# Performance work log

Measured on AMD Instinct MI355X. Metric: run time of the kernel, lower is better.

Reference implementation:

```python
import jax, jax.numpy as jnp
import numpy as np

N = 50000
P = 200000
L = 6
IN_DIM = 128
OUT_DIM = 128
HEADS = 4


def setup_inputs() -> dict:
    key = jax.random.key(0)
    ks = jax.random.split(key, 7)
    x = jax.random.normal(ks[0], (N, IN_DIM), dtype=jnp.float32)
    path_list = jax.random.randint(ks[1], (P, L), 0, N, dtype=jnp.int64)
    s = 0.1
    w_ih = jax.random.normal(ks[2], (3 * OUT_DIM, IN_DIM), dtype=jnp.float32) * s
    w_hh = jax.random.normal(ks[3], (3 * OUT_DIM, OUT_DIM), dtype=jnp.float32) * s
    b_ih = jax.random.normal(ks[4], (3 * OUT_DIM,), dtype=jnp.float32) * s
    b_hh = jax.random.normal(ks[5], (3 * OUT_DIM,), dtype=jnp.float32) * s
    a = jax.random.uniform(ks[6], (OUT_DIM, HEADS), dtype=jnp.float32) * 2.0 - 1.0
    return {"x": x, "path_list": path_list, "w_ih": w_ih, "w_hh": w_hh,
            "b_ih": b_ih, "b_hh": b_hh, "a": a}


def _gru_final_hidden(feats, w_ih, w_hh, b_ih, b_hh):
    # feats: [P, L, in_dim]; PyTorch GRU cell semantics, h0 = 0.
    out_dim = w_hh.shape[1]
    p = feats.shape[0]

    def step(h, xt):
        gi = xt @ w_ih.T + b_ih          # [P, 3*out]
        gh = h @ w_hh.T + b_hh           # [P, 3*out]
        ir, iz, i_n = jnp.split(gi, 3, axis=-1)
        hr, hz, h_n = jnp.split(gh, 3, axis=-1)
        r = jax.nn.sigmoid(ir + hr)
        z = jax.nn.sigmoid(iz + hz)
        n_cand = jnp.tanh(i_n + r * h_n)
        h_new = (1.0 - z) * n_cand + z * h
        return h_new, None

    h0 = jnp.zeros((p, out_dim), feats.dtype)
    xs = jnp.swapaxes(feats, 0, 1)       # [L, P, in_dim]
    h, _ = jax.lax.scan(step, h0, xs)
    return h                              # [P, out_dim]


def reference(x, path_list, w_ih, w_hh, b_ih, b_hh, a):
    n, out_dim = x.shape[0], w_hh.shape[1]
    heads = a.shape[1]
    # F.embedding(path_list, x): gather path features [P, L, in_dim]
    feats = x[path_list]
    path_emb = _gru_final_hidden(feats, w_ih, w_hh, b_ih, b_hh)       # [P, out]
    # unnormalized attention per head
    att_un = jnp.exp(jax.nn.leaky_relu(path_emb @ a, negative_slope=0.2))  # [P, H]
    row = path_list[:, -1]                                             # owner node of each path
    # M @ att_un : segment-sum over owner nodes
    att_sum = jax.ops.segment_sum(att_un, row, num_segments=n)         # [N, H]
    # M.t() @ (1/att_sum) : gather back to paths
    att_low = (1.0 / att_sum)[row]                                     # [P, H]
    att_n = att_un * att_low                                           # [P, H]
    # reshape(-1,1).repeat(1,out).reshape(P,-1): each head's scalar repeated out_dim times
    att_rep = jnp.repeat(att_n, out_dim, axis=1)                       # [P, H*out]
    emb_rep = jnp.tile(path_emb, (1, heads))                           # [P, H*out]
    path_att_emb = att_rep * emb_rep
    node_att_emb = jax.ops.segment_sum(path_att_emb, row, num_segments=n)  # [N, H*out]
    return node_att_emb
```

## Files before the change

### kernel.cpp

```cpp
#include <hip/hip_runtime.h>
#include <hip/hip_bf16.h>
#include <math.h>

#define NN 50000
#define PP 200000
#define LL 6
#define DD 128
#define HH 4

#define TM 64
#define NT 512
#define HPAD 132

typedef __attribute__((ext_vector_type(8))) short short8;
typedef __attribute__((ext_vector_type(4))) float f32x4;

__device__ __forceinline__ unsigned short f2bf(float v) {
    __hip_bfloat16 h = __float2bfloat16(v);
    return *(unsigned short*)&h;
}
__device__ __forceinline__ float bf2f(unsigned short u) {
    union { unsigned int i; float f; } c; c.i = ((unsigned int)u) << 16; return c.f;
}
__device__ __forceinline__ float fast_rcp(float x) { return __builtin_amdgcn_rcpf(x); }
__device__ __forceinline__ float fast_sigmoid(float x) {
    return fast_rcp(1.f + __expf(-x));
}
__device__ __forceinline__ float fast_tanh(float x) {
    float e = __expf(-2.f * fabsf(x));
    float t = (1.f - e) * fast_rcp(1.f + e);
    return copysignf(t, x);
}

__global__ void prep_x_kernel(const float* __restrict__ x,
                              unsigned short* __restrict__ xb) {
    int i = blockIdx.x * 256 + threadIdx.x;
    if (i < NN * DD) xb[i] = f2bf(x[i]);
}
__global__ void prep_w_kernel(const float* __restrict__ w_ih,
                              const float* __restrict__ w_hh,
                              unsigned short* __restrict__ wib,
                              unsigned short* __restrict__ whb) {
    int i = blockIdx.x * 256 + threadIdx.x;
    if (i < 3 * DD * DD) { wib[i] = f2bf(w_ih[i]); whb[i] = f2bf(w_hh[i]); }
}

__global__ void histo_kernel(const int* __restrict__ path_list,
                             int* __restrict__ cnt) {
    int p = blockIdx.x * 256 + threadIdx.x;
    if (p < PP) atomicAdd(&cnt[path_list[p * LL + (LL - 1)]], 1);
}

__global__ void scan_kernel(const int* __restrict__ cnt,
                            int* __restrict__ offs,
                            int* __restrict__ cursor) {
    __shared__ int ls[256];
    const int t = threadIdx.x;
    const int chunk = (NN + 255) / 256;
    int s = 0;
    for (int j = 0; j < chunk; ++j) {
        int i = t + j * 256;
        if (i < NN) s += cnt[i];
    }
    ls[t] = s; __syncthreads();
    for (int off = 1; off < 256; off <<= 1) {
        int v = (t >= off) ? ls[t - off] : 0;
        __syncthreads();
        ls[t] += v;
        __syncthreads();
    }
    int run = (t == 0) ? 0 : ls[t - 1];
    for (int j = 0; j < chunk; ++j) {
        int i = t + j * 256;
        if (i < NN) { offs[i] = run; cursor[i] = run; run += cnt[i]; }
    }
}

__global__ void scatter_kernel(const int* __restrict__ path_list,
                               int* __restrict__ cursor,
                               int* __restrict__ sorted) {
    int p = blockIdx.x * 256 + threadIdx.x;
    if (p < PP) {
        int row = path_list[p * LL + (LL - 1)];
        int k = atomicAdd(&cursor[row], 1);
        sorted[k] = p;
    }
}

__global__ __launch_bounds__(NT, 2)
void gru_att_kernel(const unsigned short* __restrict__ xb,
                    const int*   __restrict__ path_list,
                    const unsigned short* __restrict__ wib,
                    const unsigned short* __restrict__ whb,
                    const float* __restrict__ b_ih,
                    const float* __restrict__ b_hh,
                    const float* __restrict__ a,
                    float* __restrict__ att_sum,
                    unsigned short* __restrict__ emb,
                    float* __restrict__ att_un_g)
{
    __shared__ __align__(16) unsigned char smem[43520];
    unsigned short* hsb    = (unsigned short*)smem;
    unsigned short* xs     = (unsigned short*)(smem + 16384);
    float*          hs_f   = (float*)smem;
    float*          red_s  = (float*)(smem + 33792);
    int*            nodes_s= (int*)(smem + 41984);

    const int tid  = threadIdx.x;
    const int lane = tid & 63;
    const int wave = tid >> 6;
    const int lcol = lane & 15;
    const int quad = lane >> 4;
    const int d    = wave * 16 + lcol;
    const int p0   = blockIdx.x * TM;
    const int ko   = quad * 8;

    short8 Bx[3][4], Bh[3][4];
    #pragma unroll
    for (int c = 0; c < 3; ++c)
        #pragma unroll
        for (int ks = 0; ks < 4; ++ks) {
            Bx[c][ks] = *(const short8*)(wib + (size_t)(c * DD + d) * DD + ks * 32 + ko);
            Bh[c][ks] = *(const short8*)(whb + (size_t)(c * DD + d) * DD + ks * 32 + ko);
        }
    const float brz = b_ih[d]       + b_hh[d];
    const float bzz = b_ih[d + 128] + b_hh[d + 128];
    const float bin = b_ih[d + 256];
    const float bhn = b_hh[d + 256];

    for (int i = tid; i < TM * LL; i += NT) nodes_s[i] = path_list[(size_t)p0 * LL + i];
    for (int i = tid; i < TM * DD / 8; i += NT)
        ((uint4*)hsb)[i] = make_uint4(0u, 0u, 0u, 0u);

    float hreg[16];
    #pragma unroll
    for (int i = 0; i < 16; ++i) hreg[i] = 0.f;

    __syncthreads();

    const int gpi = tid >> 3;
    const int gtt = tid & 7;
    const int gpm = gpi & 15;

    uint4 xg0, xg1;
    {
        int node = nodes_s[gpi * LL + 0];
        const uint4* src = (const uint4*)(xb + (size_t)node * DD + gtt * 16);
        xg0 = src[0]; xg1 = src[1];
    }

    f32x4 accR[4], accZ[4], accN[4], accH[4];

    #pragma unroll
    for (int t = 0; t < LL; ++t) {
        {
            int kb0 = 2 * gtt, kb1 = 2 * gtt + 1;
            *(uint4*)(xs + gpi * DD + ((kb0 ^ gpm) * 8)) = xg0;
            *(uint4*)(xs + gpi * DD + ((kb1 ^ gpm) * 8)) = xg1;
        }
        __syncthreads();

        if (t < LL - 1) {
            int node = nodes_s[gpi * LL + t + 1];
            const uint4* src = (const uint4*)(xb + (size_t)node * DD + gtt * 16);
            xg0 = src[0]; xg1 = src[1];
        }

        #pragma unroll
        for (int rt = 0; rt < 4; ++rt) {
            accR[rt] = (f32x4){brz, brz, brz, brz};
            accZ[rt] = (f32x4){bzz, bzz, bzz, bzz};
            accN[rt] = (f32x4){bin, bin, bin, bin};
            accH[rt] = (f32x4){bhn, bhn, bhn, bhn};
        }

        #pragma unroll
        for (int ks = 0; ks < 4; ++ks) {
            const int kb = ks * 4 + quad;
            #pragma unroll
            for (int rt = 0; rt < 4; ++rt) {
                const int p = rt * 16 + lcol;
                short8 ax = *(const short8*)(xs  + p * DD + ((kb ^ lcol) * 8));
                short8 ah = *(const short8*)(hsb + p * DD + ((kb ^ lcol) * 8));
                accR[rt] = __builtin_amdgcn_mfma_f32_16x16x32_bf16(ax, Bx[0][ks], accR[rt], 0, 0, 0);
                accZ[rt] = __builtin_amdgcn_mfma_f32_16x16x32_bf16(ax, Bx[1][ks], accZ[rt], 0, 0, 0);
                accN[rt] = __builtin_amdgcn_mfma_f32_16x16x32_bf16(ax, Bx[2][ks], accN[rt], 0, 0, 0);
                accR[rt] = __builtin_amdgcn_mfma_f32_16x16x32_bf16(ah, Bh[0][ks], accR[rt], 0, 0, 0);
                accZ[rt] = __builtin_amdgcn_mfma_f32_16x16x32_bf16(ah, Bh[1][ks], accZ[rt], 0, 0, 0);
                accH[rt] = __builtin_amdgcn_mfma_f32_16x16x32_bf16(ah, Bh[2][ks], accH[rt], 0, 0, 0);
            }
        }
        __syncthreads();

        #pragma unroll
        for (int rt = 0; rt < 4; ++rt) {
            #pragma unroll
            for (int r = 0; r < 4; ++r) {
                const int idx = rt * 4 + r;
                const int p   = rt * 16 + quad * 4 + r;
                float rg = fast_sigmoid(accR[rt][r]);
                float zg = fast_sigmoid(accZ[rt][r]);
                float ng = fast_tanh(accN[rt][r] + rg * accH[rt][r]);
                float hnew = fmaf(zg, hreg[idx] - ng, ng);
                hreg[idx] = hnew;
                if (t < LL - 1) {
                    hsb[p * DD + (((d >> 3) ^ (p & 15)) * 8) + (d & 7)] = f2bf(hnew);
                } else {
                    hs_f[p * HPAD + d] = hnew;
                }
            }
        }
    }

    __syncthreads();

    {
        int pi = tid >> 3, tt = tid & 7;
        float s0 = 0.f, s1 = 0.f, s2 = 0.f, s3 = 0.f;
        unsigned short pack[16];
        #pragma unroll
        for (int j = 0; j < 16; ++j) {
            int dd2 = tt * 16 + j;
            float hv = hs_f[pi * HPAD + dd2];
            pack[j] = f2bf(hv);
            float4 av = *(const float4*)(a + dd2 * 4);
            s0 += hv * av.x; s1 += hv * av.y; s2 += hv * av.z; s3 += hv * av.w;
        }
        uint4* dst = (uint4*)(emb + (size_t)(p0 + pi) * DD + tt * 16);
        dst[0] = *(uint4*)&pack[0];
        dst[1] = *(uint4*)&pack[8];
        float* rp = red_s + (pi * 8 + tt) * 4;
        rp[0] = s0; rp[1] = s1; rp[2] = s2; rp[3] = s3;
    }
    __syncthreads();
    if (tid < TM) {
        int pi = tid;
        int row = nodes_s[pi * LL + (LL - 1)];
        float4 e4;
        #pragma unroll
        for (int h = 0; h < HH; ++h) {
            float s = 0.f;
            #pragma unroll
            for (int tt = 0; tt < 8; ++tt) s += red_s[(pi * 8 + tt) * 4 + h];
            float lv = (s > 0.f) ? s : 0.2f * s;
            float e  = __expf(lv);
            ((float*)&e4)[h] = e;
            atomicAdd(&att_sum[row * HH + h], e);
        }
        *(float4*)(att_un_g + (size_t)(p0 + pi) * HH) = e4;
    }
}

__global__ __launch_bounds__(256)
void agg_kernel(const unsigned short* __restrict__ emb,
                const float* __restrict__ att_un,
                const float* __restrict__ att_sum,
                const int* __restrict__ offs,
                const int* __restrict__ cnt,
                const int* __restrict__ sorted,
                float* __restrict__ out)
{
    int node = blockIdx.x * 2 + (threadIdx.x >> 7);
    int d    = threadIdx.x & 127;
    if (node >= NN) return;
    int start = offs[node];
    int len   = cnt[node];
    float a0 = 0.f, a1 = 0.f, a2 = 0.f, a3 = 0.f;
    for (int i = 0; i < len; ++i) {
        int p = sorted[start + i];
        float4 at = *(const float4*)(att_un + (size_t)p * 4);
        float ev = bf2f(emb[(size_t)p * DD + d]);
        a0 = fmaf(at.x, ev, a0);
        a1 = fmaf(at.y, ev, a1);
        a2 = fmaf(at.z, ev, a2);
        a3 = fmaf(at.w, ev, a3);
    }
    float4 s = *(const float4*)(att_sum + (size_t)node * 4);
    float* o = out + (size_t)node * 512 + d;
    o[0]   = (s.x > 0.f) ? a0 / s.x : 0.f;
    o[128] = (s.y > 0.f) ? a1 / s.y : 0.f;
    o[256] = (s.z > 0.f) ? a2 / s.z : 0.f;
    o[384] = (s.w > 0.f) ? a3 / s.w : 0.f;
}

extern "C" void kernel_launch(void* const* d_in, const int* in_sizes, int n_in,
                              void* d_out, int out_size, void* d_ws, size_t ws_size,
                              hipStream_t stream) {
    const float* x         = (const float*)d_in[0];
    const int*   path_list = (const int*)  d_in[1];
    const float* w_ih      = (const float*)d_in[2];
    const float* w_hh      = (const float*)d_in[3];
    const float* b_ih      = (const float*)d_in[4];
    const float* b_hh      = (const float*)d_in[5];
    const float* a         = (const float*)d_in[6];
    float* out = (float*)d_out;

    char* w = (char*)d_ws;
    float*          att_sum = (float*)w;                 w += 800000;
    int*            cnt     = (int*)w;                   w += 200000;
    int*            offs    = (int*)w;                   w += 200000;
    int*            cursor  = (int*)w;                   w += 200000;
    int*            sorted  = (int*)w;                   w += 800000;
    float*          att_un  = (float*)w;                 w += 3200000;
    unsigned short* xb      = (unsigned short*)w;        w += 12800000;
    unsigned short* wib     = (unsigned short*)w;        w += 98304;
    unsigned short* whb     = (unsigned short*)w;        w += 98304;
    unsigned short* emb     = (unsigned short*)w;        w += 51200000;

    hipMemsetAsync(att_sum, 0, 800000, stream);
    hipMemsetAsync(cnt, 0, 200000, stream);

    prep_x_kernel<<<(NN * DD + 255) / 256, 256, 0, stream>>>(x, xb);
    prep_w_kernel<<<(3 * DD * DD + 255) / 256, 256, 0, stream>>>(w_ih, w_hh, wib, whb);

    histo_kernel<<<(PP + 255) / 256, 256, 0, stream>>>(path_list, cnt);
    scan_kernel<<<1, 256, 0, stream>>>(cnt, offs, cursor);
    scatter_kernel<<<(PP + 255) / 256, 256, 0, stream>>>(path_list, cursor, sorted);

    gru_att_kernel<<<PP / TM, NT, 0, stream>>>(xb, path_list, wib, whb,
                                               b_ih, b_hh, a, att_sum, emb, att_un);

    agg_kernel<<<(NN + 1) / 2, 256, 0, stream>>>(emb, att_un, att_sum,
                                                 offs, cnt, sorted, out);
}
```

Baseline: 657.0 us.

## Precompute per-node input gate projections and double-buffer hidden state in GRU kernel

Computes the input-to-hidden GRU projection once per node in a new MFMA GEMM kernel and stores it as fp32, so the recurrent kernel gathers precomputed gate inputs instead of raw features and runs only the hidden-state matmuls. It also double-buffers the hidden state in shared memory to remove one barrier per timestep. The trade-off is a much larger gathered footprint (384 fp32 per path step versus 128 bf16), with fine-grained, less coalesced scalar loads.

```diff
diff --git a/kernel.cpp b/kernel.cpp
--- a/kernel.cpp
+++ b/kernel.cpp
@@ -32,17 +32,10 @@
     return copysignf(t, x);
 }
 
-__global__ void prep_x_kernel(const float* __restrict__ x,
-                              unsigned short* __restrict__ xb) {
-    int i = blockIdx.x * 256 + threadIdx.x;
-    if (i < NN * DD) xb[i] = f2bf(x[i]);
-}
-__global__ void prep_w_kernel(const float* __restrict__ w_ih,
-                              const float* __restrict__ w_hh,
-                              unsigned short* __restrict__ wib,
+__global__ void prep_w_kernel(const float* __restrict__ w_hh,
                               unsigned short* __restrict__ whb) {
     int i = blockIdx.x * 256 + threadIdx.x;
-    if (i < 3 * DD * DD) { wib[i] = f2bf(w_ih[i]); whb[i] = f2bf(w_hh[i]); }
+    if (i < 3 * DD * DD) whb[i] = f2bf(w_hh[i]);
 }
 
 __global__ void histo_kernel(const int* __restrict__ path_list,
@@ -87,12 +80,77 @@
     }
 }
 
+__global__ __launch_bounds__(512, 2)
+void gi_gemm_kernel(const float* __restrict__ x,
+                    const float* __restrict__ w_ih,
+                    const float* __restrict__ b_ih,
+                    const float* __restrict__ b_hh,
+                    float* __restrict__ gi)
+{
+    const int tid  = threadIdx.x;
+    const int lane = tid & 63;
+    const int wave = tid >> 6;
+    const int lcol = lane & 15;
+    const int quad = lane >> 4;
+    const int ko   = quad * 8;
+    const int r0   = blockIdx.x * 64;
+
+    short8 B[3][4];
+    float bias[3];
+    #pragma unroll
+    for (int j = 0; j < 3; ++j) {
+        int col = wave * 48 + j * 16 + lcol;
+        #pragma unroll
+        for (int ks = 0; ks < 4; ++ks) {
+            const float* src = w_ih + (size_t)col * 128 + ks * 32 + ko;
+            short8 b;
+            #pragma unroll
+            for (int e = 0; e < 8; ++e) b[e] = (short)f2bf(src[e]);
+            B[j][ks] = b;
+        }
+        bias[j] = b_ih[col] + ((col < 256) ? b_hh[col] : 0.f);
+    }
+
+    f32x4 acc[3][4];
+    #pragma unroll
+    for (int j = 0; j < 3; ++j)
+        #pragma unroll
+        for (int rt = 0; rt < 4; ++rt)
+            acc[j][rt] = (f32x4){bias[j], bias[j], bias[j], bias[j]};
+
+    #pragma unroll
+    for (int ks = 0; ks < 4; ++ks) {
+        #pragma unroll
+        for (int rt = 0; rt < 4; ++rt) {
+            int row = r0 + rt * 16 + lcol;
+            if (row >= NN) row = NN - 1;
+            const float* src = x + (size_t)row * 128 + ks * 32 + ko;
+            short8 av;
+            #pragma unroll
+            for (int e = 0; e < 8; ++e) av[e] = (short)f2bf(src[e]);
+            acc[0][rt] = __builtin_amdgcn_mfma_f32_16x16x32_bf16(av, B[0][ks], acc[0][rt], 0, 0, 0);
+            acc[1][rt] = __builtin_amdgcn_mfma_f32_16x16x32_bf16(av, B[1][ks], acc[1][rt], 0, 0, 0);
+            acc[2][rt] = __builtin_amdgcn_mfma_f32_16x16x32_bf16(av, B[2][ks], acc[2][rt], 0, 0, 0);
+        }
+    }
+
+    #pragma unroll
+    for (int j = 0; j < 3; ++j) {
+        int col = wave * 48 + j * 16 + lcol;
+        #pragma unroll
+        for (int rt = 0; rt < 4; ++rt)
+            #pragma unroll
+            for (int rr = 0; rr < 4; ++rr) {
+                int row = r0 + rt * 16 + quad * 4 + rr;
+                if (row < NN) gi[(size_t)row * 384 + col] = acc[j][rt][rr];
+            }
+    }
+}
+
 __global__ __launch_bounds__(NT, 2)
-void gru_att_kernel(const unsigned short* __restrict__ xb,
+void gru_att_kernel(const float* __restrict__ gi,
                     const int*   __restrict__ path_list,
-                    const unsigned short* __restrict__ wib,
                     const unsigned short* __restrict__ whb,
-                    const float* __restrict__ b_ih,
                     const float* __restrict__ b_hh,
                     const float* __restrict__ a,
                     float* __restrict__ att_sum,
@@ -100,8 +158,8 @@
                     float* __restrict__ att_un_g)
 {
     __shared__ __align__(16) unsigned char smem[43520];
-    unsigned short* hsb    = (unsigned short*)smem;
-    unsigned short* xs     = (unsigned short*)(smem + 16384);
+    unsigned short* hsb0   = (unsigned short*)smem;
+    unsigned short* hsb1   = (unsigned short*)(smem + 16384);
     float*          hs_f   = (float*)smem;
     float*          red_s  = (float*)(smem + 33792);
     int*            nodes_s= (int*)(smem + 41984);
@@ -115,22 +173,17 @@
     const int p0   = blockIdx.x * TM;
     const int ko   = quad * 8;
 
-    short8 Bx[3][4], Bh[3][4];
+    short8 Bh[3][4];
     #pragma unroll
     for (int c = 0; c < 3; ++c)
         #pragma unroll
-        for (int ks = 0; ks < 4; ++ks) {
-            Bx[c][ks] = *(const short8*)(wib + (size_t)(c * DD + d) * DD + ks * 32 + ko);
+        for (int ks = 0; ks < 4; ++ks)
             Bh[c][ks] = *(const short8*)(whb + (size_t)(c * DD + d) * DD + ks * 32 + ko);
-        }
-    const float brz = b_ih[d]       + b_hh[d];
-    const float bzz = b_ih[d + 128] + b_hh[d + 128];
-    const float bin = b_ih[d + 256];
     const float bhn = b_hh[d + 256];
 
     for (int i = tid; i < TM * LL; i += NT) nodes_s[i] = path_list[(size_t)p0 * LL + i];
     for (int i = tid; i < TM * DD / 8; i += NT)
-        ((uint4*)hsb)[i] = make_uint4(0u, 0u, 0u, 0u);
+        ((uint4*)hsb0)[i] = make_uint4(0u, 0u, 0u, 0u);
 
     float hreg[16];
     #pragma unroll
@@ -138,41 +191,26 @@
 
     __syncthreads();
 
-    const int gpi = tid >> 3;
-    const int gtt = tid & 7;
-    const int gpm = gpi & 15;
-
-    uint4 xg0, xg1;
-    {
-        int node = nodes_s[gpi * LL + 0];
-        const uint4* src = (const uint4*)(xb + (size_t)node * DD + gtt * 16);
-        xg0 = src[0]; xg1 = src[1];
-    }
-
-    f32x4 accR[4], accZ[4], accN[4], accH[4];
-
-    #pragma unroll
     for (int t = 0; t < LL; ++t) {
-        {
-            int kb0 = 2 * gtt, kb1 = 2 * gtt + 1;
-            *(uint4*)(xs + gpi * DD + ((kb0 ^ gpm) * 8)) = xg0;
-            *(uint4*)(xs + gpi * DD + ((kb1 ^ gpm) * 8)) = xg1;
-        }
-        __syncthreads();
-
-        if (t < LL - 1) {
-            int node = nodes_s[gpi * LL + t + 1];
-            const uint4* src = (const uint4*)(xb + (size_t)node * DD + gtt * 16);
-            xg0 = src[0]; xg1 = src[1];
-        }
-
-        #pragma unroll
-        for (int rt = 0; rt < 4; ++rt) {
-            accR[rt] = (f32x4){brz, brz, brz, brz};
-            accZ[rt] = (f32x4){bzz, bzz, bzz, bzz};
-            accN[rt] = (f32x4){bin, bin, bin, bin};
+        unsigned short* hr = (t & 1) ? hsb1 : hsb0;
+        unsigned short* hw = (t & 1) ? hsb0 : hsb1;
+
+        float gin[16];
+        f32x4 accR[4], accZ[4], accH[4];
+        #pragma unroll
+        for (int rt = 0; rt < 4; ++rt)
+            #pragma unroll
+            for (int r = 0; r < 4; ++r) {
+                const int p = rt * 16 + quad * 4 + r;
+                const int node = nodes_s[p * LL + t];
+                const float* g = gi + (size_t)node * 384 + d;
+                accR[rt][r] = g[0];
+                accZ[rt][r] = g[128];
+                gin[rt * 4 + r] = g[256];
+            }
+        #pragma unroll
+        for (int rt = 0; rt < 4; ++rt)
             accH[rt] = (f32x4){bhn, bhn, bhn, bhn};
-        }
 
         #pragma unroll
         for (int ks = 0; ks < 4; ++ks) {
@@ -180,17 +218,14 @@
             #pragma unroll
             for (int rt = 0; rt < 4; ++rt) {
                 const int p = rt * 16 + lcol;
-                short8 ax = *(const short8*)(xs  + p * DD + ((kb ^ lcol) * 8));
-                short8 ah = *(const short8*)(hsb + p * DD + ((kb ^ lcol) * 8));
-                accR[rt] = __builtin_amdgcn_mfma_f32_16x16x32_bf16(ax, Bx[0][ks], accR[rt], 0, 0, 0);
-                accZ[rt] = __builtin_amdgcn_mfma_f32_16x16x32_bf16(ax, Bx[1][ks], accZ[rt], 0, 0, 0);
-                accN[rt] = __builtin_amdgcn_mfma_f32_16x16x32_bf16(ax, Bx[2][ks], accN[rt], 0, 0, 0);
+                short8 ah = *(const short8*)(hr + p * DD + ((kb ^ lcol) * 8));
                 accR[rt] = __builtin_amdgcn_mfma_f32_16x16x32_bf16(ah, Bh[0][ks], accR[rt], 0, 0, 0);
                 accZ[rt] = __builtin_amdgcn_mfma_f32_16x16x32_bf16(ah, Bh[1][ks], accZ[rt], 0, 0, 0);
                 accH[rt] = __builtin_amdgcn_mfma_f32_16x16x32_bf16(ah, Bh[2][ks], accH[rt], 0, 0, 0);
             }
         }
-        __syncthreads();
+
+        if (t == LL - 1) __syncthreads();
 
         #pragma unroll
         for (int rt = 0; rt < 4; ++rt) {
@@ -200,19 +235,18 @@
                 const int p   = rt * 16 + quad * 4 + r;
                 float rg = fast_sigmoid(accR[rt][r]);
                 float zg = fast_sigmoid(accZ[rt][r]);
-                float ng = fast_tanh(accN[rt][r] + rg * accH[rt][r]);
+                float ng = fast_tanh(gin[idx] + rg * accH[rt][r]);
                 float hnew = fmaf(zg, hreg[idx] - ng, ng);
                 hreg[idx] = hnew;
                 if (t < LL - 1) {
-                    hsb[p * DD + (((d >> 3) ^ (p & 15)) * 8) + (d & 7)] = f2bf(hnew);
+                    hw[p * DD + (((d >> 3) ^ (p & 15)) * 8) + (d & 7)] = f2bf(hnew);
                 } else {
                     hs_f[p * HPAD + d] = hnew;
                 }
             }
         }
-    }
-
-    __syncthreads();
+        __syncthreads();
+    }
 
     {
         int pi = tid >> 3, tt = tid & 7;
@@ -302,23 +336,23 @@
     int*            cursor  = (int*)w;                   w += 200000;
     int*            sorted  = (int*)w;                   w += 800000;
     float*          att_un  = (float*)w;                 w += 3200000;
-    unsigned short* xb      = (unsigned short*)w;        w += 12800000;
-    unsigned short* wib     = (unsigned short*)w;        w += 98304;
+    float*          gi      = (float*)w;                 w += 76800000;
     unsigned short* whb     = (unsigned short*)w;        w += 98304;
     unsigned short* emb     = (unsigned short*)w;        w += 51200000;
 
     hipMemsetAsync(att_sum, 0, 800000, stream);
     hipMemsetAsync(cnt, 0, 200000, stream);
 
-    prep_x_kernel<<<(NN * DD + 255) / 256, 256, 0, stream>>>(x, xb);
-    prep_w_kernel<<<(3 * DD * DD + 255) / 256, 256, 0, stream>>>(w_ih, w_hh, wib, whb);
+    prep_w_kernel<<<(3 * DD * DD + 255) / 256, 256, 0, stream>>>(w_hh, whb);
 
     histo_kernel<<<(PP + 255) / 256, 256, 0, stream>>>(path_list, cnt);
     scan_kernel<<<1, 256, 0, stream>>>(cnt, offs, cursor);
     scatter_kernel<<<(PP + 255) / 256, 256, 0, stream>>>(path_list, cursor, sorted);
 
-    gru_att_kernel<<<PP / TM, NT, 0, stream>>>(xb, path_list, wib, whb,
-                                               b_ih, b_hh, a, att_sum, emb, att_un);
+    gi_gemm_kernel<<<(NN + 63) / 64, 512, 0, stream>>>(x, w_ih, b_ih, b_hh, gi);
+
+    gru_att_kernel<<<PP / TM, NT, 0, stream>>>(gi, path_list, whb,
+                                               b_hh, a, att_sum, emb, att_un);
 
     agg_kernel<<<(NN + 1) / 2, 256, 0, stream>>>(emb, att_un, att_sum,
                                                  offs, cnt, sorted, out);
```

Result: slower. 724.8 us (+10.3%).
